# Performance work log

Measured on AMD Instinct MI355X. Metric: run time of the kernel, lower is better.

The kernel has to match this reference:

```python
import jax, jax.numpy as jnp
import numpy as np

KEHALF = 7.199822675975274  # half Coulomb constant, eV*Angstrom/e^2
SR_CUTOFF = 4.0
LR_CUTOFF = 10.0
N_ATOMS = 262144
N_PAIRS = 16777216


def setup_inputs() -> dict:
    key = jax.random.key(0)
    k1, k2, k3, k4 = jax.random.split(key, 4)
    # distances in (0.1, 12.1) Angstrom: spans both cutoffs, avoids r=0 singularity
    Dij = jax.random.uniform(k1, (N_PAIRS,), dtype=jnp.float32) * 12.0 + 0.1
    Qa = jax.random.normal(k2, (N_ATOMS,), dtype=jnp.float32) * 0.3  # partial charges
    idx_i = jax.random.randint(k3, (N_PAIRS,), 0, N_ATOMS, dtype=jnp.int64)
    idx_j = jax.random.randint(k4, (N_PAIRS,), 0, N_ATOMS, dtype=jnp.int64)
    return {"Dij": Dij, "Qa": Qa, "idx_i": idx_i, "idx_j": idx_j}


def _poly_cutoff(r, cutoff):
    x = r / cutoff
    return jnp.where(x < 1.0, 1.0 - x * x * x * (x * (6.0 * x - 15.0) + 10.0), 0.0)


def reference(Dij, Qa, idx_i, idx_j):
    lr2 = LR_CUTOFF * LR_CUTOFF
    Qi = Qa[idx_i]                      # [P]
    Qj = Qa[idx_j]                      # [P]
    Dij_sh = jnp.sqrt(Dij * Dij + 1.0)  # shielded distance
    switch = _poly_cutoff(Dij, SR_CUTOFF / 2.0)  # phi(2r) with cutoff sr
    cswitch = 1.0 - switch
    E_ord = 1.0 / Dij + Dij / lr2 - 2.0 / LR_CUTOFF
    E_sh = 1.0 / Dij_sh + Dij_sh / lr2 - 2.0 / LR_CUTOFF
    Eele = KEHALF * Qi * Qj * (switch * E_sh + cswitch * E_ord)
    Eele = jnp.where(Dij <= LR_CUTOFF, Eele, 0.0)
    # scatter-add per-pair energies to atoms
    return jax.ops.segment_sum(Eele, idx_i, num_segments=Qa.shape[0])
```

## Files before the change

kernel.cpp:

```cpp
#include <hip/hip_runtime.h>


#define KEHALF 7.199822675975274f
#define NB    128
#define BSH   11
#define BMASK 2047
#define CAP   126976
#define CURSTRIDE 16
#define SCH   2
#define SCAP  72
#define VSCALE 524288.0f
#define VINV   (1.0f / 524288.0f)
#define P1B   512
#define P1PAIRS 8192

__device__ __forceinline__ float radial_fast(float d) {
    float d2p1 = d * d + 1.0f;
    float rsq  = __builtin_amdgcn_rsqf(d2p1);
    float x    = 0.5f * d;
    float sw   = (x < 1.0f) ? 1.0f - x * x * x * (x * (6.0f * x - 15.0f) + 10.0f)
                            : 0.0f;
    float Eo = __builtin_amdgcn_rcpf(d) + d * 0.01f - 0.2f;
    float Es = rsq * (1.0f + 0.01f * d2p1) - 0.2f;
    return sw * Es + (1.0f - sw) * Eo;
}

__global__ __launch_bounds__(P1B, 4) void ee_bin(
    const float* __restrict__ Dij,
    const float* __restrict__ Qa,
    const int*   __restrict__ idx_i,
    const int*   __restrict__ idx_j,
    unsigned int* __restrict__ list,
    unsigned int* __restrict__ gcur,
    float*        __restrict__ out)
{
    __shared__ unsigned int stage[NB * SCAP];
    __shared__ int lcur[NB];
    __shared__ int gofs[NB];
    int tid = threadIdx.x;
    if (tid < NB) lcur[tid] = 0;
    __syncthreads();

    long blockBase = (long)blockIdx.x * P1PAIRS;

    float D[16];
    int   II[16];
    float QJ[16];

#pragma unroll
    for (int g = 0; g < 4; ++g) {
        long o = blockBase + ((long)(g * P1B + tid)) * 4;
        int4 j4 = *reinterpret_cast<const int4*>(idx_j + o);
        QJ[g * 4 + 0] = Qa[j4.x];
        QJ[g * 4 + 1] = Qa[j4.y];
        QJ[g * 4 + 2] = Qa[j4.z];
        QJ[g * 4 + 3] = Qa[j4.w];
        float4 d4 = *reinterpret_cast<const float4*>(Dij + o);
        int4   i4 = *reinterpret_cast<const int4*>(idx_i + o);
        D[g * 4 + 0] = d4.x; D[g * 4 + 1] = d4.y;
        D[g * 4 + 2] = d4.z; D[g * 4 + 3] = d4.w;
        II[g * 4 + 0] = i4.x; II[g * 4 + 1] = i4.y;
        II[g * 4 + 2] = i4.z; II[g * 4 + 3] = i4.w;
    }

#pragma unroll
    for (int m = 0; m < 16; ++m) {
        float d = D[m];
        if (d <= 10.0f) {
            float w = QJ[m] * radial_fast(d);
            int v = __float2int_rn(w * VSCALE);
            int b  = II[m] >> BSH;
            int li = II[m] & BMASK;
            int slot = atomicAdd(&lcur[b], 1);
            if (slot < SCAP) {
                stage[b * SCAP + slot] =
                    ((unsigned int)li << 21) | ((unsigned int)v & 0x1FFFFFu);
            } else {
                atomicAdd(out + II[m], KEHALF * Qa[II[m]] * w);
            }
        }
    }
    __syncthreads();

    if (tid < NB) {
        int n = lcur[tid];
        if (n > SCAP) n = SCAP;
        lcur[tid] = n;
        int padded = (n + 15) & ~15;
        gofs[tid] = (int)atomicAdd(&gcur[tid * CURSTRIDE], (unsigned int)padded);
    }
    __syncthreads();

    int wave = tid >> 6, lane = tid & 63;
    for (int b = wave; b < NB; b += (P1B / 64)) {
        int n = lcur[b];
        int padded = (n + 15) & ~15;
        int go = gofs[b];
        long rb = (long)b * CAP;
        for (int i = lane; i < padded; i += 64) {
            unsigned int val = (i < n) ? stage[b * SCAP + i] : 0u;
            int pos = go + i;
            if (pos < CAP)
                list[rb + pos] = val;
        }
    }
}

__global__ __launch_bounds__(512) void ee_acc(
    const unsigned int* __restrict__ list,
    const unsigned int* __restrict__ gcur,
    int* __restrict__ partials)
{
    __shared__ int acc[1 << BSH];
    int b = blockIdx.x / SCH;
    int s = blockIdx.x % SCH;
    int t = threadIdx.x;
#pragma unroll
    for (int r = 0; r < (1 << BSH) / 512; ++r) acc[t + r * 512] = 0;
    __syncthreads();

    int n = (int)gcur[b * CURSTRIDE];
    if (n > CAP) n = CAP;
    int nq = n >> 2;
    int per = (nq + SCH - 1) / SCH;
    int q0 = s * per;
    int q1 = q0 + per; if (q1 > nq) q1 = nq;

    const uint4* lp4 = reinterpret_cast<const uint4*>(list + (long)b * CAP);
    for (int q = q0 + t; q < q1; q += 512) {
        uint4 u4 = lp4[q];
        unsigned int us[4] = {u4.x, u4.y, u4.z, u4.w};
#pragma unroll
        for (int k = 0; k < 4; ++k) {
            unsigned int u = us[k];
            int li = (int)(u >> 21);
            int v  = ((int)(u << 11)) >> 11;
            atomicAdd(&acc[li], v);
        }
    }
    __syncthreads();

    int* pp = partials + ((long)b * SCH + s) * (1 << BSH);
#pragma unroll
    for (int r = 0; r < (1 << BSH) / 512; ++r) pp[t + r * 512] = acc[t + r * 512];
}

__global__ __launch_bounds__(256) void ee_final(
    const int* __restrict__ partials,
    const float* __restrict__ Qa,
    float* __restrict__ out, int nAtoms)
{
    int q = blockIdx.x * blockDim.x + threadIdx.x;
    int n4 = nAtoms >> 2;
    if (q >= n4) return;
    int a0 = q << 2;
    int b  = a0 >> BSH;
    int li = a0 & BMASK;
    long base = (long)(b * SCH) * (1 << BSH) + li;
    int4 s = {0, 0, 0, 0};
#pragma unroll
    for (int r = 0; r < SCH; ++r) {
        int4 p = *reinterpret_cast<const int4*>(partials + base + (long)r * (1 << BSH));
        s.x += p.x; s.y += p.y; s.z += p.z; s.w += p.w;
    }
    float4 qv = reinterpret_cast<const float4*>(Qa)[q];
    float4 sp = reinterpret_cast<const float4*>(out)[q];
    float4 o;
    o.x = KEHALF * qv.x * ((float)s.x * VINV) + sp.x;
    o.y = KEHALF * qv.y * ((float)s.y * VINV) + sp.y;
    o.z = KEHALF * qv.z * ((float)s.z * VINV) + sp.z;
    o.w = KEHALF * qv.w * ((float)s.w * VINV) + sp.w;
    reinterpret_cast<float4*>(out)[q] = o;
}

#define FP_SCALE 4194304.0f
#define FP_INV   (1.0f / 4194304.0f)

__device__ __forceinline__ float radial_exact(float d) {
    float dsh = sqrtf(d * d + 1.0f);
    float x   = 0.5f * d;
    float sw  = (x < 1.0f) ? 1.0f - x * x * x * (x * (6.0f * x - 15.0f) + 10.0f)
                           : 0.0f;
    float Eo = 1.0f / d   + d   * 0.01f - 0.2f;
    float Es = 1.0f / dsh + dsh * 0.01f - 0.2f;
    return sw * Es + (1.0f - sw) * Eo;
}

__global__ __launch_bounds__(256) void ee_pair_fix(
    const float* __restrict__ Dij,
    const float* __restrict__ Qa,
    const int*   __restrict__ idx_i,
    const int*   __restrict__ idx_j,
    int*         __restrict__ acc,
    int P)
{
    long base = ((long)blockIdx.x * blockDim.x + threadIdx.x) * 4;
    if (base >= P) return;
    float4 d4 = *reinterpret_cast<const float4*>(Dij + base);
    int4   i4 = *reinterpret_cast<const int4*>(idx_i + base);
    int4   j4 = *reinterpret_cast<const int4*>(idx_j + base);
    float D[4]  = {d4.x, d4.y, d4.z, d4.w};
    int   ii[4] = {i4.x, i4.y, i4.z, i4.w};
    int   jj[4] = {j4.x, j4.y, j4.z, j4.w};
#pragma unroll
    for (int k = 0; k < 4; ++k) {
        float d = D[k];
        if (d > 10.0f) continue;
        float e = KEHALF * Qa[ii[k]] * Qa[jj[k]] * radial_exact(d);
        atomicAdd(acc + ii[k], __float2int_rn(e * FP_SCALE));
    }
}

__global__ __launch_bounds__(256) void ee_convert(
    const int* __restrict__ acc, float* __restrict__ out, int nAtoms)
{
    int n4 = nAtoms >> 2;
    int q = blockIdx.x * blockDim.x + threadIdx.x;
    if (q >= n4) return;
    int4 a = reinterpret_cast<const int4*>(acc)[q];
    float4 o;
    o.x = (float)a.x * FP_INV;
    o.y = (float)a.y * FP_INV;
    o.z = (float)a.z * FP_INV;
    o.w = (float)a.w * FP_INV;
    reinterpret_cast<float4*>(out)[q] = o;
}

__global__ __launch_bounds__(256) void ee_pair_direct(
    const float* __restrict__ Dij,
    const float* __restrict__ Qa,
    const int*   __restrict__ idx_i,
    const int*   __restrict__ idx_j,
    float*       __restrict__ out,
    int P)
{
    long t = (long)blockIdx.x * blockDim.x + threadIdx.x;
    if (t >= P) return;
    float d = Dij[t];
    if (d > 10.0f) return;
    atomicAdd(out + idx_i[t], KEHALF * Qa[idx_i[t]] * Qa[idx_j[t]] * radial_exact(d));
}

extern "C" void kernel_launch(void* const* d_in, const int* in_sizes, int n_in,
                              void* d_out, int out_size, void* d_ws, size_t ws_size,
                              hipStream_t stream) {
    const float* Dij   = (const float*)d_in[0];
    const float* Qa    = (const float*)d_in[1];
    const int*   idx_i = (const int*)d_in[2];
    const int*   idx_j = (const int*)d_in[3];
    float*       out   = (float*)d_out;

    int P      = in_sizes[0];
    int nAtoms = in_sizes[1];

    size_t listBytes = (size_t)NB * CAP * sizeof(unsigned int);
    size_t partBytes = (size_t)NB * SCH * (1 << BSH) * sizeof(int);
    size_t curBytes  = (size_t)NB * CURSTRIDE * sizeof(unsigned int);

    if (ws_size >= listBytes + partBytes + curBytes &&
        nAtoms == NB * (1 << BSH) && (P % P1PAIRS) == 0) {
        unsigned int* list = (unsigned int*)d_ws;
        int*          part = (int*)((char*)d_ws + listBytes);
        unsigned int* gcur = (unsigned int*)((char*)d_ws + listBytes + partBytes);
        hipMemsetAsync(gcur, 0, curBytes, stream);
        hipMemsetAsync(out, 0, (size_t)out_size * sizeof(float), stream);
        int grid1 = P / P1PAIRS;
        ee_bin<<<grid1, P1B, 0, stream>>>(Dij, Qa, idx_i, idx_j, list, gcur, out);
        ee_acc<<<NB * SCH, 512, 0, stream>>>(list, gcur, part);
        ee_final<<<(nAtoms / 4 + 255) / 256, 256, 0, stream>>>(part, Qa, out, nAtoms);
    } else if (ws_size >= (size_t)nAtoms * sizeof(int) &&
               (nAtoms & 3) == 0 && (P & 3) == 0) {
        int* acc = (int*)d_ws;
        hipMemsetAsync(acc, 0, (size_t)nAtoms * sizeof(int), stream);
        int grid = (P / 4 + 255) / 256;
        ee_pair_fix<<<grid, 256, 0, stream>>>(Dij, Qa, idx_i, idx_j, acc, P);
        ee_convert<<<(nAtoms / 4 + 255) / 256, 256, 0, stream>>>(acc, out, nAtoms);
    } else {
        hipMemsetAsync(out, 0, (size_t)out_size * sizeof(float), stream);
        int grid = (P + 255) / 256;
        ee_pair_direct<<<grid, 256, 0, stream>>>(Dij, Qa, idx_i, idx_j, out, P);
    }
}
```

Before: 281.4 us.

## Hoist loads before LDS init, shrink padding, split accumulation wider, prefetch list

The binning kernel now issues all idx_j, Dij and idx_i vector loads, then the Qa gathers, before the LDS counter init and barrier, so memory latency overlaps the setup. Per-bin padding drops from 16 to 4 entries, and padding slots spread across distinct atom indices with zero value, which cuts both list traffic and LDS atomic contention on a single address. The accumulation kernel goes from 2 to 8 blocks per bin for more parallelism and software-prefetches the next uint4 from the list. The extra partials this creates add work to the final reduction, and CAP shrinks, which tightens the overflow margin.

Measured after the change: 309.6 us. +10.0%, slower.

```diff
diff --git a/kernel.cpp b/kernel.cpp
--- a/kernel.cpp
+++ b/kernel.cpp
@@ -5,9 +5,9 @@
 #define NB    128
 #define BSH   11
 #define BMASK 2047
-#define CAP   126976
+#define CAP   114688
 #define CURSTRIDE 16
-#define SCH   2
+#define SCH   8
 #define SCAP  72
 #define VSCALE 524288.0f
 #define VINV   (1.0f / 524288.0f)
@@ -38,45 +38,53 @@
     __shared__ int lcur[NB];
     __shared__ int gofs[NB];
     int tid = threadIdx.x;
+
+    long blockBase = (long)blockIdx.x * P1PAIRS;
+
+    int4 j4[4];
+#pragma unroll
+    for (int g = 0; g < 4; ++g)
+        j4[g] = *reinterpret_cast<const int4*>(
+            idx_j + blockBase + (long)(g * P1B + tid) * 4);
+    float4 d4[4];
+    int4   i4[4];
+#pragma unroll
+    for (int g = 0; g < 4; ++g) {
+        long o = blockBase + (long)(g * P1B + tid) * 4;
+        d4[g] = *reinterpret_cast<const float4*>(Dij + o);
+        i4[g] = *reinterpret_cast<const int4*>(idx_i + o);
+    }
+    float QJ[16];
+#pragma unroll
+    for (int g = 0; g < 4; ++g) {
+        QJ[g * 4 + 0] = Qa[j4[g].x];
+        QJ[g * 4 + 1] = Qa[j4[g].y];
+        QJ[g * 4 + 2] = Qa[j4[g].z];
+        QJ[g * 4 + 3] = Qa[j4[g].w];
+    }
+
     if (tid < NB) lcur[tid] = 0;
     __syncthreads();
 
-    long blockBase = (long)blockIdx.x * P1PAIRS;
-
-    float D[16];
-    int   II[16];
-    float QJ[16];
-
 #pragma unroll
     for (int g = 0; g < 4; ++g) {
-        long o = blockBase + ((long)(g * P1B + tid)) * 4;
-        int4 j4 = *reinterpret_cast<const int4*>(idx_j + o);
-        QJ[g * 4 + 0] = Qa[j4.x];
-        QJ[g * 4 + 1] = Qa[j4.y];
-        QJ[g * 4 + 2] = Qa[j4.z];
-        QJ[g * 4 + 3] = Qa[j4.w];
-        float4 d4 = *reinterpret_cast<const float4*>(Dij + o);
-        int4   i4 = *reinterpret_cast<const int4*>(idx_i + o);
-        D[g * 4 + 0] = d4.x; D[g * 4 + 1] = d4.y;
-        D[g * 4 + 2] = d4.z; D[g * 4 + 3] = d4.w;
-        II[g * 4 + 0] = i4.x; II[g * 4 + 1] = i4.y;
-        II[g * 4 + 2] = i4.z; II[g * 4 + 3] = i4.w;
-    }
-
-#pragma unroll
-    for (int m = 0; m < 16; ++m) {
-        float d = D[m];
-        if (d <= 10.0f) {
-            float w = QJ[m] * radial_fast(d);
-            int v = __float2int_rn(w * VSCALE);
-            int b  = II[m] >> BSH;
-            int li = II[m] & BMASK;
-            int slot = atomicAdd(&lcur[b], 1);
-            if (slot < SCAP) {
-                stage[b * SCAP + slot] =
-                    ((unsigned int)li << 21) | ((unsigned int)v & 0x1FFFFFu);
-            } else {
-                atomicAdd(out + II[m], KEHALF * Qa[II[m]] * w);
+        float dd[4] = {d4[g].x, d4[g].y, d4[g].z, d4[g].w};
+        int   ii[4] = {i4[g].x, i4[g].y, i4[g].z, i4[g].w};
+#pragma unroll
+        for (int k = 0; k < 4; ++k) {
+            float d = dd[k];
+            if (d <= 10.0f) {
+                float w = QJ[g * 4 + k] * radial_fast(d);
+                int v = __float2int_rn(w * VSCALE);
+                int b  = ii[k] >> BSH;
+                int li = ii[k] & BMASK;
+                int slot = atomicAdd(&lcur[b], 1);
+                if (slot < SCAP) {
+                    stage[b * SCAP + slot] =
+                        ((unsigned int)li << 21) | ((unsigned int)v & 0x1FFFFFu);
+                } else {
+                    atomicAdd(out + ii[k], KEHALF * Qa[ii[k]] * w);
+                }
             }
         }
     }
@@ -86,7 +94,7 @@
         int n = lcur[tid];
         if (n > SCAP) n = SCAP;
         lcur[tid] = n;
-        int padded = (n + 15) & ~15;
+        int padded = (n + 3) & ~3;
         gofs[tid] = (int)atomicAdd(&gcur[tid * CURSTRIDE], (unsigned int)padded);
     }
     __syncthreads();
@@ -94,11 +102,12 @@
     int wave = tid >> 6, lane = tid & 63;
     for (int b = wave; b < NB; b += (P1B / 64)) {
         int n = lcur[b];
-        int padded = (n + 15) & ~15;
+        int padded = (n + 3) & ~3;
         int go = gofs[b];
         long rb = (long)b * CAP;
         for (int i = lane; i < padded; i += 64) {
-            unsigned int val = (i < n) ? stage[b * SCAP + i] : 0u;
+            unsigned int val = (i < n) ? stage[b * SCAP + i]
+                                       : ((unsigned int)(i & BMASK) << 21);
             int pos = go + i;
             if (pos < CAP)
                 list[rb + pos] = val;
@@ -127,14 +136,27 @@
     int q1 = q0 + per; if (q1 > nq) q1 = nq;
 
     const uint4* lp4 = reinterpret_cast<const uint4*>(list + (long)b * CAP);
-    for (int q = q0 + t; q < q1; q += 512) {
-        uint4 u4 = lp4[q];
-        unsigned int us[4] = {u4.x, u4.y, u4.z, u4.w};
+    int q = q0 + t;
+    if (q < q1) {
+        uint4 u = lp4[q];
+        for (q += 512; q < q1; q += 512) {
+            uint4 nx = lp4[q];
+            unsigned int us[4] = {u.x, u.y, u.z, u.w};
+#pragma unroll
+            for (int k = 0; k < 4; ++k) {
+                unsigned int e = us[k];
+                int li = (int)(e >> 21);
+                int v  = ((int)(e << 11)) >> 11;
+                atomicAdd(&acc[li], v);
+            }
+            u = nx;
+        }
+        unsigned int us[4] = {u.x, u.y, u.z, u.w};
 #pragma unroll
         for (int k = 0; k < 4; ++k) {
-            unsigned int u = us[k];
-            int li = (int)(u >> 21);
-            int v  = ((int)(u << 11)) >> 11;
+            unsigned int e = us[k];
+            int li = (int)(e >> 21);
+            int v  = ((int)(e << 11)) >> 11;
             atomicAdd(&acc[li], v);
         }
     }
```

## Replicate per-bin list cursors to spread global atomic contention

Applied to the files above, without the earlier changes.

Splits each atom bin's global list into eight replicas, chosen by block index, each with its own cursor. This lowers contention on the per-bin global atomics in the binning kernel. Padding shrinks from 16 to 4 entries, and pad entries now point at distinct atoms to avoid LDS atomic conflicts. Each accumulation block handles one replica and software-prefetches the next uint4. Entries that spill past a replica's fixed capacity fall back to global float atomics, which could cost more if the bins are unbalanced.

Result: no change. 282.4 us (+0.3%).

```diff
diff --git a/kernel.cpp b/kernel.cpp
--- a/kernel.cpp
+++ b/kernel.cpp
@@ -5,9 +5,11 @@
 #define NB    128
 #define BSH   11
 #define BMASK 2047
-#define CAP   126976
+#define NREP  8
+#define RCAP  14304
+#define CAP   (NREP * RCAP)
 #define CURSTRIDE 16
-#define SCH   2
+#define SCH   8
 #define SCAP  72
 #define VSCALE 524288.0f
 #define VINV   (1.0f / 524288.0f)
@@ -42,6 +44,7 @@
     __syncthreads();
 
     long blockBase = (long)blockIdx.x * P1PAIRS;
+    int rep = (int)(blockIdx.x & (NREP - 1));
 
     float D[16];
     int   II[16];
@@ -86,22 +89,29 @@
         int n = lcur[tid];
         if (n > SCAP) n = SCAP;
         lcur[tid] = n;
-        int padded = (n + 15) & ~15;
-        gofs[tid] = (int)atomicAdd(&gcur[tid * CURSTRIDE], (unsigned int)padded);
+        int padded = (n + 3) & ~3;
+        gofs[tid] = (int)atomicAdd(&gcur[(tid * NREP + rep) * CURSTRIDE],
+                                   (unsigned int)padded);
     }
     __syncthreads();
 
     int wave = tid >> 6, lane = tid & 63;
     for (int b = wave; b < NB; b += (P1B / 64)) {
         int n = lcur[b];
-        int padded = (n + 15) & ~15;
+        int padded = (n + 3) & ~3;
         int go = gofs[b];
-        long rb = (long)b * CAP;
+        long rb = (long)b * CAP + (long)rep * RCAP;
         for (int i = lane; i < padded; i += 64) {
-            unsigned int val = (i < n) ? stage[b * SCAP + i] : 0u;
+            unsigned int val = (i < n) ? stage[b * SCAP + i]
+                                       : ((unsigned int)(i & BMASK) << 21);
             int pos = go + i;
-            if (pos < CAP)
+            if (pos < RCAP) {
                 list[rb + pos] = val;
+            } else if (i < n) {
+                int atom = (b << BSH) | (int)(val >> 21);
+                int v    = ((int)(val << 11)) >> 11;
+                atomicAdd(out + atom, KEHALF * Qa[atom] * ((float)v * VINV));
+            }
         }
     }
 }
@@ -112,29 +122,40 @@
     int* __restrict__ partials)
 {
     __shared__ int acc[1 << BSH];
-    int b = blockIdx.x / SCH;
-    int s = blockIdx.x % SCH;
+    int b = blockIdx.x >> 3;
+    int s = blockIdx.x & 7;
     int t = threadIdx.x;
 #pragma unroll
     for (int r = 0; r < (1 << BSH) / 512; ++r) acc[t + r * 512] = 0;
     __syncthreads();
 
-    int n = (int)gcur[b * CURSTRIDE];
-    if (n > CAP) n = CAP;
+    int n = (int)gcur[(b * NREP + s) * CURSTRIDE];
+    if (n > RCAP) n = RCAP;
     int nq = n >> 2;
-    int per = (nq + SCH - 1) / SCH;
-    int q0 = s * per;
-    int q1 = q0 + per; if (q1 > nq) q1 = nq;
-
-    const uint4* lp4 = reinterpret_cast<const uint4*>(list + (long)b * CAP);
-    for (int q = q0 + t; q < q1; q += 512) {
-        uint4 u4 = lp4[q];
-        unsigned int us[4] = {u4.x, u4.y, u4.z, u4.w};
+
+    const uint4* lp4 =
+        reinterpret_cast<const uint4*>(list + (long)b * CAP + (long)s * RCAP);
+    int q = t;
+    if (q < nq) {
+        uint4 u = lp4[q];
+        for (q += 512; q < nq; q += 512) {
+            uint4 nx = lp4[q];
+            unsigned int us[4] = {u.x, u.y, u.z, u.w};
+#pragma unroll
+            for (int k = 0; k < 4; ++k) {
+                unsigned int e = us[k];
+                int li = (int)(e >> 21);
+                int v  = ((int)(e << 11)) >> 11;
+                atomicAdd(&acc[li], v);
+            }
+            u = nx;
+        }
+        unsigned int us[4] = {u.x, u.y, u.z, u.w};
 #pragma unroll
         for (int k = 0; k < 4; ++k) {
-            unsigned int u = us[k];
-            int li = (int)(u >> 21);
-            int v  = ((int)(u << 11)) >> 11;
+            unsigned int e = us[k];
+            int li = (int)(e >> 21);
+            int v  = ((int)(e << 11)) >> 11;
             atomicAdd(&acc[li], v);
         }
     }
@@ -255,7 +276,7 @@
 
     size_t listBytes = (size_t)NB * CAP * sizeof(unsigned int);
     size_t partBytes = (size_t)NB * SCH * (1 << BSH) * sizeof(int);
-    size_t curBytes  = (size_t)NB * CURSTRIDE * sizeof(unsigned int);
+    size_t curBytes  = (size_t)NB * NREP * CURSTRIDE * sizeof(unsigned int);
 
     if (ws_size >= listBytes + partBytes + curBytes &&
         nAtoms == NB * (1 << BSH) && (P % P1PAIRS) == 0) {
```

## Replace binning pipeline with replicated global integer atomic accumulators

Applied to the files above, without the earlier changes.

Drops the three-stage LDS bin, global list and per-bin accumulate pipeline. Each pair now does an integer atomicAdd directly into one of 8 replicated per-atom accumulator arrays, chosen by block index, and a final kernel sums the replicas and scales by the charge. This removes the list write and re-read traffic and two kernel phases. In exchange it sends one random global atomic per pair (about 14M) and adds a memset of 8 accumulator arrays.

Result: slower. 659.9 us (+134.5%).

```diff
diff --git a/kernel.cpp b/kernel.cpp
--- a/kernel.cpp
+++ b/kernel.cpp
@@ -2,17 +2,9 @@
 
 
 #define KEHALF 7.199822675975274f
-#define NB    128
-#define BSH   11
-#define BMASK 2047
-#define CAP   126976
-#define CURSTRIDE 16
-#define SCH   2
-#define SCAP  72
+#define NREPA  8
 #define VSCALE 524288.0f
 #define VINV   (1.0f / 524288.0f)
-#define P1B   512
-#define P1PAIRS 8192
 
 __device__ __forceinline__ float radial_fast(float d) {
     float d2p1 = d * d + 1.0f;
@@ -25,156 +17,58 @@
     return sw * Es + (1.0f - sw) * Eo;
 }
 
-__global__ __launch_bounds__(P1B, 4) void ee_bin(
+__global__ __launch_bounds__(256) void ee_pair_rep(
     const float* __restrict__ Dij,
     const float* __restrict__ Qa,
     const int*   __restrict__ idx_i,
     const int*   __restrict__ idx_j,
-    unsigned int* __restrict__ list,
-    unsigned int* __restrict__ gcur,
-    float*        __restrict__ out)
+    int*         __restrict__ acc,
+    int nAtoms)
 {
-    __shared__ unsigned int stage[NB * SCAP];
-    __shared__ int lcur[NB];
-    __shared__ int gofs[NB];
-    int tid = threadIdx.x;
-    if (tid < NB) lcur[tid] = 0;
-    __syncthreads();
+    long base = ((long)blockIdx.x * blockDim.x + threadIdx.x) * 4;
+    int* accr = acc + (long)(blockIdx.x & (NREPA - 1)) * nAtoms;
 
-    long blockBase = (long)blockIdx.x * P1PAIRS;
+    float4 d4 = *reinterpret_cast<const float4*>(Dij + base);
+    int4   i4 = *reinterpret_cast<const int4*>(idx_i + base);
+    int4   j4 = *reinterpret_cast<const int4*>(idx_j + base);
 
-    float D[16];
-    int   II[16];
-    float QJ[16];
+    float qj0 = Qa[j4.x], qj1 = Qa[j4.y], qj2 = Qa[j4.z], qj3 = Qa[j4.w];
 
+    float D[4]  = {d4.x, d4.y, d4.z, d4.w};
+    int   ii[4] = {i4.x, i4.y, i4.z, i4.w};
+    float QJ[4] = {qj0, qj1, qj2, qj3};
 #pragma unroll
-    for (int g = 0; g < 4; ++g) {
-        long o = blockBase + ((long)(g * P1B + tid)) * 4;
-        int4 j4 = *reinterpret_cast<const int4*>(idx_j + o);
-        QJ[g * 4 + 0] = Qa[j4.x];
-        QJ[g * 4 + 1] = Qa[j4.y];
-        QJ[g * 4 + 2] = Qa[j4.z];
-        QJ[g * 4 + 3] = Qa[j4.w];
-        float4 d4 = *reinterpret_cast<const float4*>(Dij + o);
-        int4   i4 = *reinterpret_cast<const int4*>(idx_i + o);
-        D[g * 4 + 0] = d4.x; D[g * 4 + 1] = d4.y;
-        D[g * 4 + 2] = d4.z; D[g * 4 + 3] = d4.w;
-        II[g * 4 + 0] = i4.x; II[g * 4 + 1] = i4.y;
-        II[g * 4 + 2] = i4.z; II[g * 4 + 3] = i4.w;
-    }
-
-#pragma unroll
-    for (int m = 0; m < 16; ++m) {
-        float d = D[m];
+    for (int k = 0; k < 4; ++k) {
+        float d = D[k];
         if (d <= 10.0f) {
-            float w = QJ[m] * radial_fast(d);
-            int v = __float2int_rn(w * VSCALE);
-            int b  = II[m] >> BSH;
-            int li = II[m] & BMASK;
-            int slot = atomicAdd(&lcur[b], 1);
-            if (slot < SCAP) {
-                stage[b * SCAP + slot] =
-                    ((unsigned int)li << 21) | ((unsigned int)v & 0x1FFFFFu);
-            } else {
-                atomicAdd(out + II[m], KEHALF * Qa[II[m]] * w);
-            }
-        }
-    }
-    __syncthreads();
-
-    if (tid < NB) {
-        int n = lcur[tid];
-        if (n > SCAP) n = SCAP;
-        lcur[tid] = n;
-        int padded = (n + 15) & ~15;
-        gofs[tid] = (int)atomicAdd(&gcur[tid * CURSTRIDE], (unsigned int)padded);
-    }
-    __syncthreads();
-
-    int wave = tid >> 6, lane = tid & 63;
-    for (int b = wave; b < NB; b += (P1B / 64)) {
-        int n = lcur[b];
-        int padded = (n + 15) & ~15;
-        int go = gofs[b];
-        long rb = (long)b * CAP;
-        for (int i = lane; i < padded; i += 64) {
-            unsigned int val = (i < n) ? stage[b * SCAP + i] : 0u;
-            int pos = go + i;
-            if (pos < CAP)
-                list[rb + pos] = val;
+            float w = QJ[k] * radial_fast(d);
+            atomicAdd(accr + ii[k], __float2int_rn(w * VSCALE));
         }
     }
 }
 
-__global__ __launch_bounds__(512) void ee_acc(
-    const unsigned int* __restrict__ list,
-    const unsigned int* __restrict__ gcur,
-    int* __restrict__ partials)
-{
-    __shared__ int acc[1 << BSH];
-    int b = blockIdx.x / SCH;
-    int s = blockIdx.x % SCH;
-    int t = threadIdx.x;
-#pragma unroll
-    for (int r = 0; r < (1 << BSH) / 512; ++r) acc[t + r * 512] = 0;
-    __syncthreads();
-
-    int n = (int)gcur[b * CURSTRIDE];
-    if (n > CAP) n = CAP;
-    int nq = n >> 2;
-    int per = (nq + SCH - 1) / SCH;
-    int q0 = s * per;
-    int q1 = q0 + per; if (q1 > nq) q1 = nq;
-
-    const uint4* lp4 = reinterpret_cast<const uint4*>(list + (long)b * CAP);
-    for (int q = q0 + t; q < q1; q += 512) {
-        uint4 u4 = lp4[q];
-        unsigned int us[4] = {u4.x, u4.y, u4.z, u4.w};
-#pragma unroll
-        for (int k = 0; k < 4; ++k) {
-            unsigned int u = us[k];
-            int li = (int)(u >> 21);
-            int v  = ((int)(u << 11)) >> 11;
-            atomicAdd(&acc[li], v);
-        }
-    }
-    __syncthreads();
-
-    int* pp = partials + ((long)b * SCH + s) * (1 << BSH);
-#pragma unroll
-    for (int r = 0; r < (1 << BSH) / 512; ++r) pp[t + r * 512] = acc[t + r * 512];
-}
-
-__global__ __launch_bounds__(256) void ee_final(
-    const int* __restrict__ partials,
+__global__ __launch_bounds__(256) void ee_final_rep(
+    const int* __restrict__ acc,
     const float* __restrict__ Qa,
     float* __restrict__ out, int nAtoms)
 {
     int q = blockIdx.x * blockDim.x + threadIdx.x;
     int n4 = nAtoms >> 2;
     if (q >= n4) return;
-    int a0 = q << 2;
-    int b  = a0 >> BSH;
-    int li = a0 & BMASK;
-    long base = (long)(b * SCH) * (1 << BSH) + li;
     int4 s = {0, 0, 0, 0};
 #pragma unroll
-    for (int r = 0; r < SCH; ++r) {
-        int4 p = *reinterpret_cast<const int4*>(partials + base + (long)r * (1 << BSH));
+    for (int r = 0; r < NREPA; ++r) {
+        int4 p = *reinterpret_cast<const int4*>(acc + (long)r * nAtoms + (q << 2));
         s.x += p.x; s.y += p.y; s.z += p.z; s.w += p.w;
     }
     float4 qv = reinterpret_cast<const float4*>(Qa)[q];
-    float4 sp = reinterpret_cast<const float4*>(out)[q];
     float4 o;
-    o.x = KEHALF * qv.x * ((float)s.x * VINV) + sp.x;
-    o.y = KEHALF * qv.y * ((float)s.y * VINV) + sp.y;
-    o.z = KEHALF * qv.z * ((float)s.z * VINV) + sp.z;
-    o.w = KEHALF * qv.w * ((float)s.w * VINV) + sp.w;
+    o.x = KEHALF * qv.x * ((float)s.x * VINV);
+    o.y = KEHALF * qv.y * ((float)s.y * VINV);
+    o.z = KEHALF * qv.z * ((float)s.z * VINV);
+    o.w = KEHALF * qv.w * ((float)s.w * VINV);
     reinterpret_cast<float4*>(out)[q] = o;
 }
-
-#define FP_SCALE 4194304.0f
-#define FP_INV   (1.0f / 4194304.0f)
 
 __device__ __forceinline__ float radial_exact(float d) {
     float dsh = sqrtf(d * d + 1.0f);
@@ -184,46 +78,6 @@
     float Eo = 1.0f / d   + d   * 0.01f - 0.2f;
     float Es = 1.0f / dsh + dsh * 0.01f - 0.2f;
     return sw * Es + (1.0f - sw) * Eo;
-}
-
-__global__ __launch_bounds__(256) void ee_pair_fix(
-    const float* __restrict__ Dij,
-    const float* __restrict__ Qa,
-    const int*   __restrict__ idx_i,
-    const int*   __restrict__ idx_j,
-    int*         __restrict__ acc,
-    int P)
-{
-    long base = ((long)blockIdx.x * blockDim.x + threadIdx.x) * 4;
-    if (base >= P) return;
-    float4 d4 = *reinterpret_cast<const float4*>(Dij + base);
-    int4   i4 = *reinterpret_cast<const int4*>(idx_i + base);
-    int4   j4 = *reinterpret_cast<const int4*>(idx_j + base);
-    float D[4]  = {d4.x, d4.y, d4.z, d4.w};
-    int   ii[4] = {i4.x, i4.y, i4.z, i4.w};
-    int   jj[4] = {j4.x, j4.y, j4.z, j4.w};
-#pragma unroll
-    for (int k = 0; k < 4; ++k) {
-        float d = D[k];
-        if (d > 10.0f) continue;
-        float e = KEHALF * Qa[ii[k]] * Qa[jj[k]] * radial_exact(d);
-        atomicAdd(acc + ii[k], __float2int_rn(e * FP_SCALE));
-    }
-}
-
-__global__ __launch_bounds__(256) void ee_convert(
-    const int* __restrict__ acc, float* __restrict__ out, int nAtoms)
-{
-    int n4 = nAtoms >> 2;
-    int q = blockIdx.x * blockDim.x + threadIdx.x;
-    if (q >= n4) return;
-    int4 a = reinterpret_cast<const int4*>(acc)[q];
-    float4 o;
-    o.x = (float)a.x * FP_INV;
-    o.y = (float)a.y * FP_INV;
-    o.z = (float)a.z * FP_INV;
-    o.w = (float)a.w * FP_INV;
-    reinterpret_cast<float4*>(out)[q] = o;
 }
 
 __global__ __launch_bounds__(256) void ee_pair_direct(
@@ -253,28 +107,15 @@
     int P      = in_sizes[0];
     int nAtoms = in_sizes[1];
 
-    size_t listBytes = (size_t)NB * CAP * sizeof(unsigned int);
-    size_t partBytes = (size_t)NB * SCH * (1 << BSH) * sizeof(int);
-    size_t curBytes  = (size_t)NB * CURSTRIDE * sizeof(unsigned int);
+    size_t accBytes = (size_t)NREPA * nAtoms * sizeof(int);
 
-    if (ws_size >= listBytes + partBytes + curBytes &&
-        nAtoms == NB * (1 << BSH) && (P % P1PAIRS) == 0) {
-        unsigned int* list = (unsigned int*)d_ws;
-        int*          part = (int*)((char*)d_ws + listBytes);
-        unsigned int* gcur = (unsigned int*)((char*)d_ws + listBytes + partBytes);
-        hipMemsetAsync(gcur, 0, curBytes, stream);
-        hipMemsetAsync(out, 0, (size_t)out_size * sizeof(float), stream);
-        int grid1 = P / P1PAIRS;
-        ee_bin<<<grid1, P1B, 0, stream>>>(Dij, Qa, idx_i, idx_j, list, gcur, out);
-        ee_acc<<<NB * SCH, 512, 0, stream>>>(list, gcur, part);
-        ee_final<<<(nAtoms / 4 + 255) / 256, 256, 0, stream>>>(part, Qa, out, nAtoms);
-    } else if (ws_size >= (size_t)nAtoms * sizeof(int) &&
-               (nAtoms & 3) == 0 && (P & 3) == 0) {
+    if (ws_size >= accBytes && (P % 1024) == 0 && (nAtoms & 3) == 0) {
         int* acc = (int*)d_ws;
-        hipMemsetAsync(acc, 0, (size_t)nAtoms * sizeof(int), stream);
-        int grid = (P / 4 + 255) / 256;
-        ee_pair_fix<<<grid, 256, 0, stream>>>(Dij, Qa, idx_i, idx_j, acc, P);
-        ee_convert<<<(nAtoms / 4 + 255) / 256, 256, 0, stream>>>(acc, out, nAtoms);
+        hipMemsetAsync(acc, 0, accBytes, stream);
+        int grid = P / 1024;
+        ee_pair_rep<<<grid, 256, 0, stream>>>(Dij, Qa, idx_i, idx_j, acc, nAtoms);
+        ee_final_rep<<<(nAtoms / 4 + 255) / 256, 256, 0, stream>>>(acc, Qa, out,
+                                                                   nAtoms);
     } else {
         hipMemsetAsync(out, 0, (size_t)out_size * sizeof(float), stream);
         int grid = (P + 255) / 256;
```
